# Optimization experiments

Measured on AMD Instinct MI355X. Metric: run time of the kernel, lower is better.

The kernel has to match this reference:

```python
import jax, jax.numpy as jnp
import numpy as np

N = 2048
GRID = 125
G3 = GRID ** 3
DX = 10.0 / GRID
INV_DX = 1.0 / DX
DENSITY = 1000.0
DT0 = 0.0417

_OFF = np.array([[i, j, k] for i in range(3) for j in range(3) for k in range(3)], dtype=np.int32)  # 27 stencil offsets


def setup_inputs() -> dict:
    key = jax.random.key(0)
    k1, k2, k3, k4 = jax.random.split(key, 4)
    bs, T = 2, 16
    x = jax.random.uniform(k1, (bs, T, N, 3), dtype=jnp.float32)
    vol = jax.random.uniform(k2, (bs, N), dtype=jnp.float32)
    F = jax.random.normal(k3, (bs, T, N, 3, 3), dtype=jnp.float32)
    C = jax.random.normal(k4, (bs, T, N, 3, 3), dtype=jnp.float32)
    return {"x": x, "vol": vol, "F": F, "C": C, "frame_interval": 2, "norm_fac": 5}


def reference(x, vol, F, C, frame_interval, norm_fac):
    if norm_fac > 0:
        x = x * 2 + norm_fac
    dT = DT0 * frame_interval
    bs, T = x.shape[0], x.shape[1]
    start_t = 1 if frame_interval == 1 else 0
    end_t = T - 2
    M = bs * (end_t - start_t)

    px = x[:, start_t:end_t].reshape(M, N, 3)
    pv = ((x[:, start_t + 2:end_t + 2] - x[:, start_t:end_t]) / (2 * dT)).reshape(M, N, 3)
    pF = F[:, start_t:end_t].reshape(M, N, 3, 3)
    pFn = F[:, start_t + 1:end_t + 1].reshape(M, N, 3, 3)
    pC = C[:, start_t:end_t].reshape(M, N, 3, 3)
    mass = DENSITY * jnp.repeat(vol[:, None], end_t - start_t, axis=1).reshape(M, N)  # [M,N]

    gp = px * INV_DX
    base = (gp - 0.5).astype(jnp.int32)            # positions are positive -> trunc == floor
    fx = gp - base                                  # [M,N,3]
    # quadratic B-spline weights, axis-major: w[..., axis, offset]
    w = jnp.stack([0.5 * (1.5 - fx) ** 2, 0.75 - (fx - 1) ** 2, 0.5 * (fx - 0.5) ** 2], axis=-1)
    dw = jnp.stack([fx - 1.5, -2 * (fx - 1), fx - 0.5], axis=-1)

    off = jnp.asarray(_OFF)                         # [27,3]
    wi = w[:, :, 0, off[:, 0]]; wj = w[:, :, 1, off[:, 1]]; wk = w[:, :, 2, off[:, 2]]
    dwi = dw[:, :, 0, off[:, 0]]; dwj = dw[:, :, 1, off[:, 1]]; dwk = dw[:, :, 2, off[:, 2]]
    weight = wi * wj * wk                           # [M,N,27]
    dweight = jnp.stack([dwi * wj * wk, wi * dwj * wk, wi * wj * dwk], axis=-1) * INV_DX  # [M,N,27,3]

    node = base[:, :, None, :] + off[None, None]    # [M,N,27,3]
    flat = (node[..., 0] * GRID + node[..., 1]) * GRID + node[..., 2]  # [M,N,27]

    dpos = (off[None, None].astype(fx.dtype) - fx[:, :, None, :]) * DX  # [M,N,27,3]
    vel = pv[:, :, None, :] + jnp.einsum('mnab,mnob->mnoa', pC, dpos)   # APIC velocity
    mw = mass[:, :, None] * weight                  # [M,N,27]
    v_in = mw[..., None] * vel                      # [M,N,27,3]

    midx = jnp.arange(M)[:, None, None]
    grid_v = jnp.zeros((M, G3, 3), x.dtype).at[midx, flat].add(v_in)   # P2G momentum scatter
    grid_m = jnp.zeros((M, G3), x.dtype).at[midx, flat].add(mw)        # P2G mass scatter
    grid_m = jnp.where(grid_m > 1e-15, grid_m, jnp.ones_like(grid_m))
    grid_v = grid_v / grid_m[..., None]

    gv = grid_v[midx, flat]                          # G2P gather [M,N,27,3]
    new_F = jnp.einsum('mnoa,mnob->mnab', gv, dweight)  # velocity gradient
    I3 = jnp.eye(3, dtype=x.dtype)
    F_pred = jnp.einsum('mnab,mnbc->mnac', I3 + new_F * dT, pF)
    return jnp.mean(jnp.abs(F_pred - pFn)) * (end_t - start_t)
```

## Files before the change

kernel.cpp:

```cpp
#include <hip/hip_runtime.h>

constexpr float DT0      = 0.0417f;
constexpr float DENSITY_ = 1000.0f;
constexpr float DXF      = 10.0f / 125.0f;
constexpr float INV_DXF  = 12.5f;

constexpr int DIM  = 32;
constexpr int DIM2 = DIM * DIM;

constexpr int SLAB    = 4;
constexpr int PLN     = 6;
constexpr int NSLAB   = 8;
constexpr int THREADS = 1024;
constexpr int QPC     = 2048;
constexpr int QGC     = 1024;

constexpr float MSCALE = 262144.0f;
constexpr float PSCALE = 4096.0f;
constexpr float VOFF   = 32.0f;

using u32 = unsigned int;
using u64 = unsigned long long;

__device__ __forceinline__ int window_min(int nf) {
    int b = 0;
    if (nf > 0) {
        b = (int)(12.5f * (float)nf - 0.5f) - 2;
        if (b < 0) b = 0;
    }
    return b;
}

__global__ __launch_bounds__(THREADS)
void fused_kernel(const float* __restrict__ x,
                  const float* __restrict__ vol,
                  const float* __restrict__ F,
                  const float* __restrict__ C,
                  const int* __restrict__ fi_p,
                  const int* __restrict__ nf_p,
                  float* __restrict__ out,
                  int bs, int T, int Np)
{
    __shared__ u64 acc[PLN * DIM2 * 2];
    __shared__ unsigned short qp[QPC];
    __shared__ unsigned short qg[QGC];
    __shared__ int cnt[2];
    __shared__ float wsum[THREADS / 64];

    const int fi = fi_p[0], nf = nf_p[0];
    const int start_t = (fi == 1) ? 1 : 0;
    const int TS = (T - 2) - start_t;
    const int M  = bs * TS;

    const int m    = blockIdx.x >> 3;
    const int slab = blockIdx.x & (NSLAB - 1);
    const int s4   = slab * SLAB;
    const int tid  = threadIdx.x;
    const int lane = tid & 63;

    if (tid < 2) cnt[tid] = 0;
    __syncthreads();

    const int bmin = window_min(nf);
    const float nff = (float)nf;
    const float dT = DT0 * (float)fi;
    const float inv2dT = 1.0f / (2.0f * dT);

    int b = 0, t = 0;
    const float* x0s = nullptr;
    const float* x2s = nullptr;
    const float* Cs  = nullptr;
    const float* vs  = nullptr;
    if (m < M) {
        b = m / TS;
        t = (m - b * TS) + start_t;
        x0s = x + (((size_t)b * T + t)     * Np) * 3;
        x2s = x + (((size_t)b * T + t + 2) * Np) * 3;
        Cs  = C + (((size_t)b * T + t)     * Np) * 9;
        vs  = vol + (size_t)b * Np;
    }

    for (int i = tid; i < PLN * DIM2 * 2; i += THREADS) acc[i] = 0ull;

    if (m < M) {
        for (int n = tid; n < Np; n += THREADS) {
            float a0 = x0s[3 * n];
            if (nf > 0) a0 = a0 * 2.0f + nff;
            const float gp0 = a0 * INV_DXF;
            const int b0 = (int)(gp0 - 0.5f);
            const int l0 = b0 - bmin;
            const int rel = l0 - s4 + 2;
            const bool mP = ((unsigned)rel < 8u);
            const int l0loc = l0 - s4;
            const bool mG = ((unsigned)l0loc < (unsigned)SLAB);

            unsigned long long mk = __ballot(mP);
            if (mk) {
                const int leader = __ffsll(mk) - 1;
                const int pre = __popcll(mk & ((1ull << lane) - 1ull));
                int base = 0;
                if (lane == leader) base = atomicAdd(&cnt[0], __popcll(mk));
                base = __shfl(base, leader, 64);
                if (mP && base + pre < QPC)
                    qp[base + pre] = (unsigned short)(n | (rel << 11));
            }
            mk = __ballot(mG);
            if (mk) {
                const int leader = __ffsll(mk) - 1;
                const int pre = __popcll(mk & ((1ull << lane) - 1ull));
                int base = 0;
                if (lane == leader) base = atomicAdd(&cnt[1], __popcll(mk));
                base = __shfl(base, leader, 64);
                if (mG && base + pre < QGC)
                    qg[base + pre] = (unsigned short)(n | (l0loc << 11));
            }
        }
    }
    __syncthreads();

    if (m < M) {
        const int np2g = min(cnt[0], QPC);
        for (int e = tid; e < np2g; e += THREADS) {
            const int ent = qp[e];
            const int n   = ent & 2047;
            const int rel = ent >> 11;

            float a0 = x0s[3 * n], a1 = x0s[3 * n + 1], a2 = x0s[3 * n + 2];
            float c0 = x2s[3 * n], c1 = x2s[3 * n + 1], c2 = x2s[3 * n + 2];
            const float mass = DENSITY_ * vs[n];
            float Cm[9];
#pragma unroll
            for (int r = 0; r < 9; ++r) Cm[r] = Cs[9 * n + r];

            if (nf > 0) {
                a0 = a0 * 2.0f + nff; a1 = a1 * 2.0f + nff; a2 = a2 * 2.0f + nff;
                c0 = c0 * 2.0f + nff; c1 = c1 * 2.0f + nff; c2 = c2 * 2.0f + nff;
            }
            const float gp0 = a0 * INV_DXF;
            const int   b0  = (int)(gp0 - 0.5f);
            const float fx0 = gp0 - (float)b0;
            const float gp1 = a1 * INV_DXF;
            const int   b1  = (int)(gp1 - 0.5f);
            const float fx1 = gp1 - (float)b1;
            const float gp2 = a2 * INV_DXF;
            const int   b2  = (int)(gp2 - 0.5f);
            const float fx2 = gp2 - (float)b2;
            const int l1 = b1 - bmin, l2 = b2 - bmin;

            const float pv0 = (c0 - a0) * inv2dT;
            const float pv1 = (c1 - a1) * inv2dT;
            const float pv2 = (c2 - a2) * inv2dT;

            float w0a[3], w1a[3], w2a[3];
            w0a[0] = 0.5f * (1.5f - fx0) * (1.5f - fx0);
            w0a[1] = 0.75f - (fx0 - 1.0f) * (fx0 - 1.0f);
            w0a[2] = 0.5f * (fx0 - 0.5f) * (fx0 - 0.5f);
            w1a[0] = 0.5f * (1.5f - fx1) * (1.5f - fx1);
            w1a[1] = 0.75f - (fx1 - 1.0f) * (fx1 - 1.0f);
            w1a[2] = 0.5f * (fx1 - 0.5f) * (fx1 - 0.5f);
            w2a[0] = 0.5f * (1.5f - fx2) * (1.5f - fx2);
            w2a[1] = 0.75f - (fx2 - 1.0f) * (fx2 - 1.0f);
            w2a[2] = 0.5f * (fx2 - 0.5f) * (fx2 - 0.5f);

            const float dpx0 = (-fx0) * DXF;
            const float dpy0 = (-fx1) * DXF;
            const float dpz0 = (-fx2) * DXF;
            float vix = pv0 + Cm[0]*dpx0 + Cm[1]*dpy0 + Cm[2]*dpz0;
            float viy = pv1 + Cm[3]*dpx0 + Cm[4]*dpy0 + Cm[5]*dpz0;
            float viz = pv2 + Cm[6]*dpx0 + Cm[7]*dpy0 + Cm[8]*dpz0;
            const float dix = Cm[0] * DXF, diy = Cm[3] * DXF, diz = Cm[6] * DXF;
            const float djx = Cm[1] * DXF, djy = Cm[4] * DXF, djz = Cm[7] * DXF;
            const float dkx = Cm[2] * DXF, dky = Cm[5] * DXF, dkz = Cm[8] * DXF;

            const bool fastp = (l1 >= 0 && l1 <= DIM - 3 &&
                                l2 >= 0 && l2 <= DIM - 3);
            int lp = rel - 2;
#pragma unroll
            for (int i = 0; i < 3; ++i) {
                if ((unsigned)lp < (unsigned)PLN) {
                    const float wim = mass * w0a[i];
                    u64* pb = acc + lp * (DIM2 * 2);
                    float vjx = vix, vjy = viy, vjz = viz;
#pragma unroll
                    for (int j = 0; j < 3; ++j) {
                        const int lj = fastp ? (l1 + j)
                                             : min(max(l1 + j, 0), DIM - 1);
                        const float wijm = wim * w1a[j];
                        float vx = vjx, vy = vjy, vz = vjz;
#pragma unroll
                        for (int k = 0; k < 3; ++k) {
                            const int lk = fastp ? (l2 + k)
                                                 : min(max(l2 + k, 0), DIM - 1);
                            const float mw = wijm * w2a[k];
                            const float pm = mw * PSCALE;
                            const u32 am = (u32)(mw * MSCALE);
                            const u32 ix = (u32)(int)(pm * vx);
                            const u32 iy = (u32)(int)(pm * vy);
                            const u32 iz = (u32)(int)(pm * (vz + VOFF));
                            u64* cp = pb + (lj * DIM + lk) * 2;
                            atomicAdd(cp + 0, ((u64)ix << 32) | (u64)am);
                            atomicAdd(cp + 1, ((u64)iy << 32) | (u64)iz);
                            vx += dkx; vy += dky; vz += dkz;
                        }
                        vjx += djx; vjy += djy; vjz += djz;
                    }
                }
                vix += dix; viy += diy; viz += diz;
                ++lp;
            }
        }
    }
    __syncthreads();

    for (int c = tid; c < PLN * DIM2; c += THREADS) {
        const u64 A = acc[c * 2 + 0];
        const u64 B = acc[c * 2 + 1];
        const u32 mass_u = (u32)A;
        const int momx = (int)(u32)(A >> 32);
        const int momy = (int)(u32)(B >> 32);
        const int momz = (int)((u32)B - (mass_u >> 1));
        const float inv = (mass_u != 0u) ? 64.0f / (float)mass_u
                                         : (1.0f / 4096.0f);
        ((float4*)acc)[c] = make_float4((float)momx * inv,
                                        (float)momy * inv,
                                        (float)momz * inv, 0.0f);
    }
    __syncthreads();

    float s = 0.0f;
    if (m < M) {
        const int ng = min(cnt[1], QGC);
        const int q  = tid & 3;
        const float4* vel = (const float4*)acc;
        for (int e = tid >> 2; e < ng; e += THREADS / 4) {
            const int ent   = qg[e];
            const int n     = ent & 2047;
            const int l0loc = ent >> 11;

            float a0 = x0s[3 * n], a1 = x0s[3 * n + 1], a2 = x0s[3 * n + 2];
            if (nf > 0) {
                a0 = a0 * 2.0f + nff; a1 = a1 * 2.0f + nff; a2 = a2 * 2.0f + nff;
            }
            float fxv[3]; int lb1, lb2;
            {
                const float gp0 = a0 * INV_DXF;
                const int   b0  = (int)(gp0 - 0.5f);
                fxv[0] = gp0 - (float)b0;
                const float gp1 = a1 * INV_DXF;
                const int   b1  = (int)(gp1 - 0.5f);
                fxv[1] = gp1 - (float)b1;
                const float gp2 = a2 * INV_DXF;
                const int   b2  = (int)(gp2 - 0.5f);
                fxv[2] = gp2 - (float)b2;
                lb1 = b1 - bmin; lb2 = b2 - bmin;
            }
            float w[3][3], dw[3][3];
#pragma unroll
            for (int d = 0; d < 3; ++d) {
                w[d][0] = 0.5f * (1.5f - fxv[d]) * (1.5f - fxv[d]);
                w[d][1] = 0.75f - (fxv[d] - 1.0f) * (fxv[d] - 1.0f);
                w[d][2] = 0.5f * (fxv[d] - 0.5f) * (fxv[d] - 0.5f);
                dw[d][0] = fxv[d] - 1.5f;
                dw[d][1] = -2.0f * (fxv[d] - 1.0f);
                dw[d][2] = fxv[d] - 0.5f;
            }

            float nF[9] = {0,0,0,0,0,0,0,0,0};
#pragma unroll
            for (int o = q; o < 27; o += 4) {
                const int i = o / 9, j = (o / 3) % 3, k = o % 3;
                const int lp = min(max(l0loc + i, 0), PLN - 1);
                const int lj = min(max(lb1 + j, 0), DIM - 1);
                const int lk = min(max(lb2 + k, 0), DIM - 1);
                const float4 g = vel[lp * DIM2 + lj * DIM + lk];
                const float dwx = dw[0][i] *  w[1][j] *  w[2][k] * INV_DXF;
                const float dwy =  w[0][i] * dw[1][j] *  w[2][k] * INV_DXF;
                const float dwz =  w[0][i] *  w[1][j] * dw[2][k] * INV_DXF;
                nF[0] += g.x * dwx; nF[1] += g.x * dwy; nF[2] += g.x * dwz;
                nF[3] += g.y * dwx; nF[4] += g.y * dwy; nF[5] += g.y * dwz;
                nF[6] += g.z * dwx; nF[7] += g.z * dwy; nF[8] += g.z * dwz;
            }
#pragma unroll
            for (int d = 1; d < 4; d <<= 1) {
#pragma unroll
                for (int r = 0; r < 9; ++r) nF[r] += __shfl_xor(nF[r], d, 64);
            }

            const float* pF  = F + (((size_t)b * T + t)     * Np + n) * 9;
            const float* pFn = F + (((size_t)b * T + t + 1) * Np + n) * 9;
            float Fm[9];
#pragma unroll
            for (int i = 0; i < 9; ++i) Fm[i] = pF[i];
#pragma unroll
            for (int ee = q; ee < 9; ee += 4) {
                const int a = ee / 3, c = ee - 3 * a;
                const float fp = Fm[a * 3 + c] + dT *
                    (nF[a * 3 + 0] * Fm[0 + c] +
                     nF[a * 3 + 1] * Fm[3 + c] +
                     nF[a * 3 + 2] * Fm[6 + c]);
                s += fabsf(fp - pFn[ee]);
            }
        }
        s *= (float)TS / ((float)M * (float)Np * 9.0f);
    }

#pragma unroll
    for (int o = 32; o > 0; o >>= 1) s += __shfl_down(s, o, 64);
    if (lane == 0) wsum[tid >> 6] = s;
    __syncthreads();
    if (tid == 0) {
        float tot = 0.0f;
#pragma unroll
        for (int w2 = 0; w2 < THREADS / 64; ++w2) tot += wsum[w2];
        atomicAdd(out, tot);
    }
}

extern "C" void kernel_launch(void* const* d_in, const int* in_sizes, int n_in,
                              void* d_out, int out_size, void* d_ws, size_t ws_size,
                              hipStream_t stream) {
    const float* x   = (const float*)d_in[0];
    const float* vol = (const float*)d_in[1];
    const float* F   = (const float*)d_in[2];
    const float* C   = (const float*)d_in[3];
    const int*   fi  = (const int*)d_in[4];
    const int*   nf  = (const int*)d_in[5];

    const int Np = 2048;
    const int bs = in_sizes[1] / Np;
    const int T  = in_sizes[0] / (bs * Np * 3);
    const int MMAX = bs * (T - 2);
    const int NBLK = MMAX * NSLAB;

    hipMemsetAsync(d_out, 0, sizeof(float), stream);

    fused_kernel<<<NBLK, THREADS, 0, stream>>>(x, vol, F, C, fi, nf,
                                               (float*)d_out, bs, T, Np);
}
```

Before: 91.26 us.

## Split each x-slab block into two y-halves to shrink shared grid tile

Each block now owns a 4-plane x-slab and half of the y range (16 owned rows plus a 2-row halo on each side), which doubles the block count. The shared accumulation tile and the particle queues shrink to match, and launch bounds now request 4 blocks per CU. The goal is higher occupancy and less per-block zeroing and conversion work. In exchange, every particle position is read and binned by twice as many blocks, and the halo rows add redundant scatter work.

```diff
diff --git a/kernel.cpp b/kernel.cpp
--- a/kernel.cpp
+++ b/kernel.cpp
@@ -6,14 +6,15 @@
 constexpr float INV_DXF  = 12.5f;
 
 constexpr int DIM  = 32;
-constexpr int DIM2 = DIM * DIM;
 
 constexpr int SLAB    = 4;
 constexpr int PLN     = 6;
-constexpr int NSLAB   = 8;
+constexpr int YOWN    = 16;
+constexpr int YROW    = 20;
+constexpr int NSUB    = 16;
 constexpr int THREADS = 1024;
-constexpr int QPC     = 2048;
-constexpr int QGC     = 1024;
+constexpr int QPC     = 1024;
+constexpr int QGC     = 512;
 
 constexpr float MSCALE = 262144.0f;
 constexpr float PSCALE = 4096.0f;
@@ -31,7 +32,7 @@
     return b;
 }
 
-__global__ __launch_bounds__(THREADS)
+__global__ __launch_bounds__(THREADS, 4)
 void fused_kernel(const float* __restrict__ x,
                   const float* __restrict__ vol,
                   const float* __restrict__ F,
@@ -41,7 +42,7 @@
                   float* __restrict__ out,
                   int bs, int T, int Np)
 {
-    __shared__ u64 acc[PLN * DIM2 * 2];
+    __shared__ u64 acc[PLN * YROW * DIM * 2];
     __shared__ unsigned short qp[QPC];
     __shared__ unsigned short qg[QGC];
     __shared__ int cnt[2];
@@ -52,9 +53,12 @@
     const int TS = (T - 2) - start_t;
     const int M  = bs * TS;
 
-    const int m    = blockIdx.x >> 3;
-    const int slab = blockIdx.x & (NSLAB - 1);
+    const int m    = blockIdx.x >> 4;
+    const int sub  = blockIdx.x & (NSUB - 1);
+    const int slab = sub >> 1;
+    const int h    = sub & 1;
     const int s4   = slab * SLAB;
+    const int yb   = h * YOWN - 2;
     const int tid  = threadIdx.x;
     const int lane = tid & 63;
 
@@ -80,19 +84,25 @@
         vs  = vol + (size_t)b * Np;
     }
 
-    for (int i = tid; i < PLN * DIM2 * 2; i += THREADS) acc[i] = 0ull;
+    for (int i = tid; i < PLN * YROW * DIM * 2; i += THREADS) acc[i] = 0ull;
 
     if (m < M) {
         for (int n = tid; n < Np; n += THREADS) {
-            float a0 = x0s[3 * n];
-            if (nf > 0) a0 = a0 * 2.0f + nff;
+            float a0 = x0s[3 * n], a1 = x0s[3 * n + 1];
+            if (nf > 0) { a0 = a0 * 2.0f + nff; a1 = a1 * 2.0f + nff; }
             const float gp0 = a0 * INV_DXF;
             const int b0 = (int)(gp0 - 0.5f);
             const int l0 = b0 - bmin;
-            const int rel = l0 - s4 + 2;
-            const bool mP = ((unsigned)rel < 8u);
+            const float gp1 = a1 * INV_DXF;
+            const int b1 = (int)(gp1 - 0.5f);
+            const int l1 = b1 - bmin;
+
+            const int rel  = l0 - s4 + 2;
+            const int yrel = l1 - yb;
+            const bool mP = ((unsigned)rel < 8u) && ((unsigned)yrel < (unsigned)YROW);
             const int l0loc = l0 - s4;
-            const bool mG = ((unsigned)l0loc < (unsigned)SLAB);
+            const bool mG = ((unsigned)l0loc < (unsigned)SLAB) &&
+                            ((unsigned)(l1 - (yb + 2)) < (unsigned)YOWN);
 
             unsigned long long mk = __ballot(mP);
             if (mk) {
@@ -146,6 +156,7 @@
             const int   b2  = (int)(gp2 - 0.5f);
             const float fx2 = gp2 - (float)b2;
             const int l1 = b1 - bmin, l2 = b2 - bmin;
+            const int r0 = l1 - yb;
 
             const float pv0 = (c0 - a0) * inv2dT;
             const float pv1 = (c1 - a1) * inv2dT;
@@ -172,35 +183,35 @@
             const float djx = Cm[1] * DXF, djy = Cm[4] * DXF, djz = Cm[7] * DXF;
             const float dkx = Cm[2] * DXF, dky = Cm[5] * DXF, dkz = Cm[8] * DXF;
 
-            const bool fastp = (l1 >= 0 && l1 <= DIM - 3 &&
-                                l2 >= 0 && l2 <= DIM - 3);
+            const bool fastz = (l2 >= 0 && l2 <= DIM - 3);
             int lp = rel - 2;
 #pragma unroll
             for (int i = 0; i < 3; ++i) {
                 if ((unsigned)lp < (unsigned)PLN) {
                     const float wim = mass * w0a[i];
-                    u64* pb = acc + lp * (DIM2 * 2);
+                    u64* pb = acc + lp * (YROW * DIM * 2);
                     float vjx = vix, vjy = viy, vjz = viz;
 #pragma unroll
                     for (int j = 0; j < 3; ++j) {
-                        const int lj = fastp ? (l1 + j)
-                                             : min(max(l1 + j, 0), DIM - 1);
-                        const float wijm = wim * w1a[j];
-                        float vx = vjx, vy = vjy, vz = vjz;
-#pragma unroll
-                        for (int k = 0; k < 3; ++k) {
-                            const int lk = fastp ? (l2 + k)
-                                                 : min(max(l2 + k, 0), DIM - 1);
-                            const float mw = wijm * w2a[k];
-                            const float pm = mw * PSCALE;
-                            const u32 am = (u32)(mw * MSCALE);
-                            const u32 ix = (u32)(int)(pm * vx);
-                            const u32 iy = (u32)(int)(pm * vy);
-                            const u32 iz = (u32)(int)(pm * (vz + VOFF));
-                            u64* cp = pb + (lj * DIM + lk) * 2;
-                            atomicAdd(cp + 0, ((u64)ix << 32) | (u64)am);
-                            atomicAdd(cp + 1, ((u64)iy << 32) | (u64)iz);
-                            vx += dkx; vy += dky; vz += dkz;
+                        const int rr = r0 + j;
+                        if ((unsigned)rr < (unsigned)YROW) {
+                            const float wijm = wim * w1a[j];
+                            float vx = vjx, vy = vjy, vz = vjz;
+#pragma unroll
+                            for (int k = 0; k < 3; ++k) {
+                                const int lk = fastz ? (l2 + k)
+                                                     : min(max(l2 + k, 0), DIM - 1);
+                                const float mw = wijm * w2a[k];
+                                const float pm = mw * PSCALE;
+                                const u32 am = (u32)(mw * MSCALE);
+                                const u32 ix = (u32)(int)(pm * vx);
+                                const u32 iy = (u32)(int)(pm * vy);
+                                const u32 iz = (u32)(int)(pm * (vz + VOFF));
+                                u64* cp = pb + (rr * DIM + lk) * 2;
+                                atomicAdd(cp + 0, ((u64)ix << 32) | (u64)am);
+                                atomicAdd(cp + 1, ((u64)iy << 32) | (u64)iz);
+                                vx += dkx; vy += dky; vz += dkz;
+                            }
                         }
                         vjx += djx; vjy += djy; vjz += djz;
                     }
@@ -212,7 +223,7 @@
     }
     __syncthreads();
 
-    for (int c = tid; c < PLN * DIM2; c += THREADS) {
+    for (int c = tid; c < PLN * YROW * DIM; c += THREADS) {
         const u64 A = acc[c * 2 + 0];
         const u64 B = acc[c * 2 + 1];
         const u32 mass_u = (u32)A;
@@ -252,7 +263,8 @@
                 const float gp2 = a2 * INV_DXF;
                 const int   b2  = (int)(gp2 - 0.5f);
                 fxv[2] = gp2 - (float)b2;
-                lb1 = b1 - bmin; lb2 = b2 - bmin;
+                lb1 = (b1 - bmin) - yb;
+                lb2 = b2 - bmin;
             }
             float w[3][3], dw[3][3];
 #pragma unroll
@@ -270,9 +282,9 @@
             for (int o = q; o < 27; o += 4) {
                 const int i = o / 9, j = (o / 3) % 3, k = o % 3;
                 const int lp = min(max(l0loc + i, 0), PLN - 1);
-                const int lj = min(max(lb1 + j, 0), DIM - 1);
+                const int lj = min(max(lb1 + j, 0), YROW - 1);
                 const int lk = min(max(lb2 + k, 0), DIM - 1);
-                const float4 g = vel[lp * DIM2 + lj * DIM + lk];
+                const float4 g = vel[(lp * YROW + lj) * DIM + lk];
                 const float dwx = dw[0][i] *  w[1][j] *  w[2][k] * INV_DXF;
                 const float dwy =  w[0][i] * dw[1][j] *  w[2][k] * INV_DXF;
                 const float dwz =  w[0][i] *  w[1][j] * dw[2][k] * INV_DXF;
@@ -330,7 +342,7 @@
     const int bs = in_sizes[1] / Np;
     const int T  = in_sizes[0] / (bs * Np * 3);
     const int MMAX = bs * (T - 2);
-    const int NBLK = MMAX * NSLAB;
+    const int NBLK = MMAX * NSUB;
 
     hipMemsetAsync(d_out, 0, sizeof(float), stream);
 
```

Result: slower. 103.2 us (+13.1%).
